# Kernel optimization log

Measured on AMD Instinct MI355X. Metric: run time of the kernel, lower is better.

The kernel has to match this reference:

```python
import jax, jax.numpy as jnp
import numpy as np

V, B, F = 4, 8192, 128  # views, batch, fea_out
EPS = 1e-5  # torch BatchNorm1d default eps


def setup_inputs() -> dict:
    key = jax.random.key(0)
    k1, k2 = jax.random.split(key)
    x = jax.random.normal(k1, (V, B, F), dtype=jnp.float32)
    # Linear(F*F -> F) weight/bias; scale ~ kaiming-ish to keep activations sane
    W = jax.random.normal(k2, (F, F * F), dtype=jnp.float32) * 0.01
    b = jnp.zeros((F,), dtype=jnp.float32)
    gamma = jnp.ones((F,), dtype=jnp.float32)   # BN weight
    beta = jnp.zeros((F,), dtype=jnp.float32)   # BN bias
    return {"x": x, "W": W, "b": b, "gamma": gamma, "beta": beta}


def reference(x, W, b, gamma, beta):
    # x: [V, B, F] stack of views. Original loops over pairs (i<j):
    #   outer = x[i][:, :, None] @ x[j][:, None, :]          -> [B, F, F]
    #   flat  = outer.view(B, F*F)   (flat index = i*F + j)
    #   out   = ReLU(BN(Linear(flat)))
    # We fuse: Linear(flat(outer)) == einsum over W reshaped to [F_out, F, F],
    # avoiding the [B, F*F] intermediate. Same math.
    Vn, Bn, Fn = x.shape
    ii, jj = np.triu_indices(Vn, k=1)          # P = V*(V-1)/2 pairs
    x1 = x[ii]                                  # [P, B, F]
    x2 = x[jj]                                  # [P, B, F]
    Wr = W.reshape(Fn, Fn, Fn)                  # [F_out, F_i, F_j], matches row-major flatten
    # bilinear form per pair/batch: y[p,b,o] = sum_ij x1[p,b,i] * Wr[o,i,j] * x2[p,b,j] + b[o]
    y = jnp.einsum('pbi,oij,pbj->pbo', x1, Wr, x2) + b
    # BatchNorm1d in training mode: per-call batch stats (over batch axis, per pair),
    # biased variance, then affine, then ReLU.
    mean = jnp.mean(y, axis=1, keepdims=True)
    var = jnp.var(y, axis=1, keepdims=True)
    y_hat = (y - mean) * jax.lax.rsqrt(var + EPS)
    out = jax.nn.relu(gamma * y_hat + beta)     # [P, B, F]
    return out
```

## Files before the change

### kernel.cpp

```cpp
#include <hip/hip_runtime.h>

#define Fdim 128
#define Bsz  8192
#define Pn   6
#define EPSI 1e-5f
#define X2P 130
#define X1P 66

typedef _Float16 half8   __attribute__((ext_vector_type(8)));
typedef _Float16 half4t  __attribute__((ext_vector_type(4)));
typedef float    float4t __attribute__((ext_vector_type(4)));
typedef float    float16t __attribute__((ext_vector_type(16)));

__constant__ int PAIR_A[6] = {0,0,0,1,1,2};
__constant__ int PAIR_B[6] = {1,2,3,2,3,3};

__global__ __launch_bounds__(256) void wprep(const float* __restrict__ W,
                                             _Float16* __restrict__ Wws) {
    int t    = blockIdx.x * 256 + threadIdx.x;
    int f    = t >> 6;
    int lane = t & 63;
    int ntile = f >> 10;
    int jc    = (f >> 7) & 7;
    int i     = f & 127;
    int q1 = lane >> 5;
    int nn = lane & 31;
    int n  = ntile * 32 + nn;
    int k0 = i * 128 + jc * 16 + q1 * 8;
    const float4t* src = (const float4t*)(W + (size_t)n * 16384 + k0);
    float4t a0 = src[0];
    float4t a1 = src[1];
    half8 h;
    h[0] = (_Float16)a0[0]; h[1] = (_Float16)a0[1];
    h[2] = (_Float16)a0[2]; h[3] = (_Float16)a0[3];
    h[4] = (_Float16)a1[0]; h[5] = (_Float16)a1[1];
    h[6] = (_Float16)a1[2]; h[7] = (_Float16)a1[3];
    *(half8*)(Wws + (size_t)t * 8) = h;
}

__global__ __launch_bounds__(256, 3) void gemm(const float* __restrict__ x,
                                               const _Float16* __restrict__ Wws,
                                               _Float16* __restrict__ yws,
                                               float* __restrict__ ssum,
                                               float* __restrict__ ssq) {
    __shared__ __align__(16) _Float16 x2t[128 * X2P];
    __shared__ __align__(16) _Float16 x1th[128 * X1P];

    int bid  = blockIdx.x;
    int p    = bid >> 7;
    int rem  = bid & 127;
    int mblk = rem >> 1;
    int nh   = rem & 1;
    int m0   = mblk * 128;
    int v1   = PAIR_A[p];
    int v2   = PAIR_B[p];
    int tid  = threadIdx.x;

    {
        const float4t* s2p = (const float4t*)(x + ((size_t)v2 * Bsz + m0) * Fdim);
        for (int it = 0; it < 16; ++it) {
            int idx = it * 256 + tid;
            int row = idx >> 5;
            int col = (idx & 31) * 4;
            float4t b = s2p[idx];
            half4t h2; h2[0]=(_Float16)b[0]; h2[1]=(_Float16)b[1];
                       h2[2]=(_Float16)b[2]; h2[3]=(_Float16)b[3];
            *(half4t*)&x2t[row * X2P + col] = h2;
        }
    }

    int lane  = tid & 63;
    int w     = tid >> 6;
    int wcol  = w & 1;
    int kw    = w >> 1;
    int nn    = lane & 31;
    int q1    = lane >> 5;
    int ntile = nh * 2 + wcol;

    float16t acc[4];
#pragma unroll
    for (int mt = 0; mt < 4; ++mt)
#pragma unroll
        for (int e = 0; e < 16; ++e)
            acc[mt][e] = 0.f;

    const half8* wb = (const half8*)Wws;
    const float* x1src = x + ((size_t)v1 * Bsz + m0) * Fdim;

    for (int kh = 0; kh < 2; ++kh) {
        if (kh) __syncthreads();
        for (int it = 0; it < 8; ++it) {
            int idx = it * 256 + tid;
            int row = idx >> 4;
            int c4  = (idx & 15) * 4;
            float4t a = *(const float4t*)(x1src + (size_t)row * Fdim + kh * 64 + c4);
            half4t h1; h1[0]=(_Float16)a[0]; h1[1]=(_Float16)a[1];
                       h1[2]=(_Float16)a[2]; h1[3]=(_Float16)a[3];
            *(half4t*)&x1th[row * X1P + c4] = h1;
        }
        __syncthreads();

#pragma unroll 1
        for (int jcl = 0; jcl < 4; ++jcl) {
            int jc = kw * 4 + jcl;
            half8 x2f[4];
#pragma unroll
            for (int mt = 0; mt < 4; ++mt)
                x2f[mt] = *(const half8*)&x2t[(mt * 32 + nn) * X2P + jc * 16 + q1 * 8];

            unsigned woff = (unsigned)((ntile * 1024 + jc * 128 + kh * 64) * 64 + lane);
            half8 wbuf[4];
#pragma unroll
            for (int d = 0; d < 4; ++d) wbuf[d] = wb[woff + d * 64];

#pragma unroll
            for (int il8 = 0; il8 < 8; ++il8) {
                half8 x1f[4];
#pragma unroll
                for (int mt = 0; mt < 4; ++mt)
                    x1f[mt] = *(const half8*)&x1th[(mt * 32 + nn) * X1P + il8 * 8];
#pragma unroll
                for (int ii = 0; ii < 8; ++ii) {
                    const int il = il8 * 8 + ii;
#pragma unroll
                    for (int mt = 0; mt < 4; ++mt) {
                        half8 a = x2f[mt] * x1f[mt][ii];
                        acc[mt] = __builtin_amdgcn_mfma_f32_32x32x16_f16(a, wbuf[il & 3], acc[mt], 0, 0, 0);
                    }
                    wbuf[il & 3] = wb[woff + (unsigned)(il + 4) * 64];
                }
                __builtin_amdgcn_sched_barrier(0);
            }
        }
    }

    __syncthreads();
    float4t* xch = (float4t*)x2t;
    if (kw == 1) {
#pragma unroll
        for (int mt = 0; mt < 4; ++mt)
#pragma unroll
            for (int r4 = 0; r4 < 4; ++r4) {
                float4t v = {acc[mt][r4*4+0], acc[mt][r4*4+1],
                             acc[mt][r4*4+2], acc[mt][r4*4+3]};
                xch[(wcol * 16 + mt * 4 + r4) * 64 + lane] = v;
            }
    }
    __syncthreads();
    if (kw == 0) {
#pragma unroll
        for (int mt = 0; mt < 4; ++mt)
#pragma unroll
            for (int r4 = 0; r4 < 4; ++r4) {
                float4t v = xch[(wcol * 16 + mt * 4 + r4) * 64 + lane];
                acc[mt][r4*4+0] += v[0]; acc[mt][r4*4+1] += v[1];
                acc[mt][r4*4+2] += v[2]; acc[mt][r4*4+3] += v[3];
            }

        float sum = 0.f, sq = 0.f;
        int colg = ntile * 32 + nn;
#pragma unroll
        for (int mt = 0; mt < 4; ++mt) {
#pragma unroll
            for (int r = 0; r < 16; ++r) {
                int rl = (r & 3) + 8 * (r >> 2) + 4 * q1;
                size_t row = (size_t)p * Bsz + m0 + mt * 32 + rl;
                float v = acc[mt][r];
                sum += v; sq += v * v;
                yws[row * Fdim + colg] = (_Float16)v;
            }
        }
        sum += __shfl_xor(sum, 32, 64);
        sq  += __shfl_xor(sq, 32, 64);
        if (q1 == 0) {
            atomicAdd(&ssum[p * Fdim + colg], sum);
            atomicAdd(&ssq [p * Fdim + colg], sq);
        }
    }
}

__global__ __launch_bounds__(256) void bnrelu(const _Float16* __restrict__ yws,
                                              const float* __restrict__ ssum,
                                              const float* __restrict__ ssq,
                                              const float* __restrict__ gamma,
                                              const float* __restrict__ beta,
                                              float* __restrict__ out) {
    __shared__ float gs[128], sh[128];
    size_t ebase = (size_t)blockIdx.x * 1024;
    int p = (int)(ebase >> 20);
    int t = threadIdx.x;
    if (t < 128) {
        float mean = ssum[p * Fdim + t] * (1.0f / 8192.0f);
        float var  = ssq [p * Fdim + t] * (1.0f / 8192.0f) - mean * mean;
        float g    = gamma[t] * rsqrtf(var + EPSI);
        gs[t] = g;
        sh[t] = beta[t] - g * mean;
    }
    __syncthreads();
    size_t e0 = ebase + (size_t)t * 4;
    int o0 = (int)(e0 & 127);
    half4t y = *(const half4t*)(yws + e0);
    float4t r;
#pragma unroll
    for (int l = 0; l < 4; ++l) {
        float v = fmaf(gs[o0 + l], (float)y[l], sh[o0 + l]);
        r[l] = v > 0.f ? v : 0.f;
    }
    *(float4t*)(out + e0) = r;
}

extern "C" void kernel_launch(void* const* d_in, const int* in_sizes, int n_in,
                              void* d_out, int out_size, void* d_ws, size_t ws_size,
                              hipStream_t stream) {
    const float* x     = (const float*)d_in[0];
    const float* W     = (const float*)d_in[1];
    const float* gamma = (const float*)d_in[3];
    const float* beta  = (const float*)d_in[4];
    float* out = (float*)d_out;

    char* ws = (char*)d_ws;
    _Float16* Wws = (_Float16*)ws;
    _Float16* yws = (_Float16*)(ws + 4194304);
    float*    ssum = (float*)(ws + 16777216);
    float*    ssq  = ssum + Pn * Fdim;

    (void)hipMemsetAsync(ssum, 0, 2 * Pn * Fdim * sizeof(float), stream);
    wprep<<<1024, 256, 0, stream>>>(W, Wws);
    gemm<<<768, 256, 0, stream>>>(x, Wws, yws, ssum, ssq);
    bnrelu<<<6144, 256, 0, stream>>>(yws, ssum, ssq, gamma, beta, out);
}
```

Baseline: 270.9 us.

## Retile GEMM warps to 2x2 MFMA blocks with packed f16 scaling

Each warp now computes a 64-row by 64-column tile (2 M-tiles x 2 N-tiles) instead of 128x32. This halves the per-MFMA A-operand construction (x2*x1 scaling) and x1/x2 LDS reads, at the cost of loading twice as many W fragments from global per warp. The scalar-broadcast multiply is done with inline v_pk_mul_f16 using op_sel to pick the halves. The separate memset of the BN statistics buffer is folded into the wprep kernel, which removes one launch.

```diff
diff --git a/kernel.cpp b/kernel.cpp
--- a/kernel.cpp
+++ b/kernel.cpp
@@ -11,12 +11,38 @@
 typedef _Float16 half4t  __attribute__((ext_vector_type(4)));
 typedef float    float4t __attribute__((ext_vector_type(4)));
 typedef float    float16t __attribute__((ext_vector_type(16)));
+typedef unsigned uint4v  __attribute__((ext_vector_type(4)));
 
 __constant__ int PAIR_A[6] = {0,0,0,1,1,2};
 __constant__ int PAIR_B[6] = {1,2,3,2,3,3};
 
+__device__ __forceinline__ half8 bmul_lo(half8 v, unsigned s) {
+    uint4v x = __builtin_bit_cast(uint4v, v);
+    unsigned r0, r1, r2, r3;
+    asm("v_pk_mul_f16 %0, %1, %2 op_sel:[0,0] op_sel_hi:[1,0]" : "=v"(r0) : "v"(x[0]), "v"(s));
+    asm("v_pk_mul_f16 %0, %1, %2 op_sel:[0,0] op_sel_hi:[1,0]" : "=v"(r1) : "v"(x[1]), "v"(s));
+    asm("v_pk_mul_f16 %0, %1, %2 op_sel:[0,0] op_sel_hi:[1,0]" : "=v"(r2) : "v"(x[2]), "v"(s));
+    asm("v_pk_mul_f16 %0, %1, %2 op_sel:[0,0] op_sel_hi:[1,0]" : "=v"(r3) : "v"(x[3]), "v"(s));
+    uint4v o = {r0, r1, r2, r3};
+    return __builtin_bit_cast(half8, o);
+}
+__device__ __forceinline__ half8 bmul_hi(half8 v, unsigned s) {
+    uint4v x = __builtin_bit_cast(uint4v, v);
+    unsigned r0, r1, r2, r3;
+    asm("v_pk_mul_f16 %0, %1, %2 op_sel:[0,1] op_sel_hi:[1,1]" : "=v"(r0) : "v"(x[0]), "v"(s));
+    asm("v_pk_mul_f16 %0, %1, %2 op_sel:[0,1] op_sel_hi:[1,1]" : "=v"(r1) : "v"(x[1]), "v"(s));
+    asm("v_pk_mul_f16 %0, %1, %2 op_sel:[0,1] op_sel_hi:[1,1]" : "=v"(r2) : "v"(x[2]), "v"(s));
+    asm("v_pk_mul_f16 %0, %1, %2 op_sel:[0,1] op_sel_hi:[1,1]" : "=v"(r3) : "v"(x[3]), "v"(s));
+    uint4v o = {r0, r1, r2, r3};
+    return __builtin_bit_cast(half8, o);
+}
+
 __global__ __launch_bounds__(256) void wprep(const float* __restrict__ W,
-                                             _Float16* __restrict__ Wws) {
+                                             _Float16* __restrict__ Wws,
+                                             float* __restrict__ stats) {
+    if (blockIdx.x == 0) {
+        for (int i = threadIdx.x; i < 2 * Pn * Fdim; i += 256) stats[i] = 0.f;
+    }
     int t    = blockIdx.x * 256 + threadIdx.x;
     int f    = t >> 6;
     int lane = t & 63;
@@ -69,23 +95,29 @@
         }
     }
 
-    int lane  = tid & 63;
-    int w     = tid >> 6;
-    int wcol  = w & 1;
-    int kw    = w >> 1;
-    int nn    = lane & 31;
-    int q1    = lane >> 5;
-    int ntile = nh * 2 + wcol;
-
-    float16t acc[4];
-#pragma unroll
-    for (int mt = 0; mt < 4; ++mt)
-#pragma unroll
-        for (int e = 0; e < 16; ++e)
-            acc[mt][e] = 0.f;
+    int lane = tid & 63;
+    int w    = __builtin_amdgcn_readfirstlane(tid >> 6);
+    int wrow = w & 1;
+    int kw   = w >> 1;
+    int nn   = lane & 31;
+    int q1   = lane >> 5;
+
+    float16t acc[2][2];
+#pragma unroll
+    for (int mt = 0; mt < 2; ++mt)
+#pragma unroll
+        for (int nt = 0; nt < 2; ++nt)
+#pragma unroll
+            for (int e = 0; e < 16; ++e)
+                acc[mt][nt][e] = 0.f;
 
     const half8* wb = (const half8*)Wws;
     const float* x1src = x + ((size_t)v1 * Bsz + m0) * Fdim;
+
+    const _Float16* x2p0 = &x2t[(wrow * 64 + nn) * X2P + q1 * 8];
+    const _Float16* x2p1 = &x2t[(wrow * 64 + 32 + nn) * X2P + q1 * 8];
+    const _Float16* x1p0 = &x1th[(wrow * 64 + nn) * X1P];
+    const _Float16* x1p1 = &x1th[(wrow * 64 + 32 + nn) * X1P];
 
     for (int kh = 0; kh < 2; ++kh) {
         if (kh) __syncthreads();
@@ -103,31 +135,39 @@
 #pragma unroll 1
         for (int jcl = 0; jcl < 4; ++jcl) {
             int jc = kw * 4 + jcl;
-            half8 x2f[4];
-#pragma unroll
-            for (int mt = 0; mt < 4; ++mt)
-                x2f[mt] = *(const half8*)&x2t[(mt * 32 + nn) * X2P + jc * 16 + q1 * 8];
-
-            unsigned woff = (unsigned)((ntile * 1024 + jc * 128 + kh * 64) * 64 + lane);
-            half8 wbuf[4];
-#pragma unroll
-            for (int d = 0; d < 4; ++d) wbuf[d] = wb[woff + d * 64];
+            half8 x2f0 = *(const half8*)(x2p0 + jc * 16);
+            half8 x2f1 = *(const half8*)(x2p1 + jc * 16);
+
+            const half8* wpA = wb + (size_t)(((nh * 2 + 0) * 1024 + jc * 128 + kh * 64) * 64);
+            const half8* wpB = wb + (size_t)(((nh * 2 + 1) * 1024 + jc * 128 + kh * 64) * 64);
+            half8 wbufA[4], wbufB[4];
+#pragma unroll
+            for (int d = 0; d < 4; ++d) {
+                wbufA[d] = wpA[lane + d * 64];
+                wbufB[d] = wpB[lane + d * 64];
+            }
 
 #pragma unroll
             for (int il8 = 0; il8 < 8; ++il8) {
-                half8 x1f[4];
-#pragma unroll
-                for (int mt = 0; mt < 4; ++mt)
-                    x1f[mt] = *(const half8*)&x1th[(mt * 32 + nn) * X1P + il8 * 8];
+                half8 x1f0 = *(const half8*)(x1p0 + il8 * 8);
+                half8 x1f1 = *(const half8*)(x1p1 + il8 * 8);
+                uint4v s0v = __builtin_bit_cast(uint4v, x1f0);
+                uint4v s1v = __builtin_bit_cast(uint4v, x1f1);
 #pragma unroll
                 for (int ii = 0; ii < 8; ++ii) {
-                    const int il = il8 * 8 + ii;
-#pragma unroll
-                    for (int mt = 0; mt < 4; ++mt) {
-                        half8 a = x2f[mt] * x1f[mt][ii];
-                        acc[mt] = __builtin_amdgcn_mfma_f32_32x32x16_f16(a, wbuf[il & 3], acc[mt], 0, 0, 0);
-                    }
-                    wbuf[il & 3] = wb[woff + (unsigned)(il + 4) * 64];
+                    const int sl = ii & 3;
+                    unsigned sd0 = s0v[ii >> 1];
+                    unsigned sd1 = s1v[ii >> 1];
+                    half8 a0, a1;
+                    if ((ii & 1) == 0) { a0 = bmul_lo(x2f0, sd0); a1 = bmul_lo(x2f1, sd1); }
+                    else               { a0 = bmul_hi(x2f0, sd0); a1 = bmul_hi(x2f1, sd1); }
+                    acc[0][0] = __builtin_amdgcn_mfma_f32_32x32x16_f16(a0, wbufA[sl], acc[0][0], 0, 0, 0);
+                    acc[0][1] = __builtin_amdgcn_mfma_f32_32x32x16_f16(a0, wbufB[sl], acc[0][1], 0, 0, 0);
+                    acc[1][0] = __builtin_amdgcn_mfma_f32_32x32x16_f16(a1, wbufA[sl], acc[1][0], 0, 0, 0);
+                    acc[1][1] = __builtin_amdgcn_mfma_f32_32x32x16_f16(a1, wbufB[sl], acc[1][1], 0, 0, 0);
+                    wbufA[sl] = wpA[lane + 256];
+                    wbufB[sl] = wpB[lane + 256];
+                    wpA += 64; wpB += 64;
                 }
                 __builtin_amdgcn_sched_barrier(0);
             }
@@ -138,43 +178,58 @@
     float4t* xch = (float4t*)x2t;
     if (kw == 1) {
 #pragma unroll
-        for (int mt = 0; mt < 4; ++mt)
-#pragma unroll
-            for (int r4 = 0; r4 < 4; ++r4) {
-                float4t v = {acc[mt][r4*4+0], acc[mt][r4*4+1],
-                             acc[mt][r4*4+2], acc[mt][r4*4+3]};
-                xch[(wcol * 16 + mt * 4 + r4) * 64 + lane] = v;
-            }
+        for (int mt = 0; mt < 2; ++mt)
+#pragma unroll
+            for (int nt = 0; nt < 2; ++nt)
+#pragma unroll
+                for (int r4 = 0; r4 < 4; ++r4) {
+                    float4t v = {acc[mt][nt][r4*4+0], acc[mt][nt][r4*4+1],
+                                 acc[mt][nt][r4*4+2], acc[mt][nt][r4*4+3]};
+                    xch[((wrow * 4 + mt * 2 + nt) * 4 + r4) * 64 + lane] = v;
+                }
     }
     __syncthreads();
     if (kw == 0) {
 #pragma unroll
-        for (int mt = 0; mt < 4; ++mt)
-#pragma unroll
-            for (int r4 = 0; r4 < 4; ++r4) {
-                float4t v = xch[(wcol * 16 + mt * 4 + r4) * 64 + lane];
-                acc[mt][r4*4+0] += v[0]; acc[mt][r4*4+1] += v[1];
-                acc[mt][r4*4+2] += v[2]; acc[mt][r4*4+3] += v[3];
-            }
-
-        float sum = 0.f, sq = 0.f;
-        int colg = ntile * 32 + nn;
-#pragma unroll
-        for (int mt = 0; mt < 4; ++mt) {
-#pragma unroll
-            for (int r = 0; r < 16; ++r) {
-                int rl = (r & 3) + 8 * (r >> 2) + 4 * q1;
-                size_t row = (size_t)p * Bsz + m0 + mt * 32 + rl;
-                float v = acc[mt][r];
-                sum += v; sq += v * v;
-                yws[row * Fdim + colg] = (_Float16)v;
-            }
-        }
-        sum += __shfl_xor(sum, 32, 64);
-        sq  += __shfl_xor(sq, 32, 64);
+        for (int mt = 0; mt < 2; ++mt)
+#pragma unroll
+            for (int nt = 0; nt < 2; ++nt)
+#pragma unroll
+                for (int r4 = 0; r4 < 4; ++r4) {
+                    float4t v = xch[((wrow * 4 + mt * 2 + nt) * 4 + r4) * 64 + lane];
+                    acc[mt][nt][r4*4+0] += v[0]; acc[mt][nt][r4*4+1] += v[1];
+                    acc[mt][nt][r4*4+2] += v[2]; acc[mt][nt][r4*4+3] += v[3];
+                }
+
+        float sum[2] = {0.f, 0.f};
+        float sq[2]  = {0.f, 0.f};
+#pragma unroll
+        for (int mt = 0; mt < 2; ++mt) {
+#pragma unroll
+            for (int nt = 0; nt < 2; ++nt) {
+                int colg = (nh * 2 + nt) * 32 + nn;
+#pragma unroll
+                for (int r = 0; r < 16; ++r) {
+                    int rl = (r & 3) + 8 * (r >> 2) + 4 * q1;
+                    size_t row = (size_t)p * Bsz + m0 + wrow * 64 + mt * 32 + rl;
+                    float v = acc[mt][nt][r];
+                    sum[nt] += v; sq[nt] += v * v;
+                    yws[row * Fdim + colg] = (_Float16)v;
+                }
+            }
+        }
+#pragma unroll
+        for (int nt = 0; nt < 2; ++nt) {
+            sum[nt] += __shfl_xor(sum[nt], 32, 64);
+            sq[nt]  += __shfl_xor(sq[nt], 32, 64);
+        }
         if (q1 == 0) {
-            atomicAdd(&ssum[p * Fdim + colg], sum);
-            atomicAdd(&ssq [p * Fdim + colg], sq);
+#pragma unroll
+            for (int nt = 0; nt < 2; ++nt) {
+                int colg = (nh * 2 + nt) * 32 + nn;
+                atomicAdd(&ssum[p * Fdim + colg], sum[nt]);
+                atomicAdd(&ssq [p * Fdim + colg], sq[nt]);
+            }
         }
     }
 }
@@ -224,8 +279,7 @@
     float*    ssum = (float*)(ws + 16777216);
     float*    ssq  = ssum + Pn * Fdim;
 
-    (void)hipMemsetAsync(ssum, 0, 2 * Pn * Fdim * sizeof(float), stream);
-    wprep<<<1024, 256, 0, stream>>>(W, Wws);
+    wprep<<<1024, 256, 0, stream>>>(W, Wws, ssum);
     gemm<<<768, 256, 0, stream>>>(x, Wws, yws, ssum, ssq);
     bnrelu<<<6144, 256, 0, stream>>>(yws, ssum, ssq, gamma, beta, out);
 }
```

Result: slower. 286.7 us (+5.8%).
